# Performance work log

Hardware: AMD Instinct MI355X
Metric: run time of the kernel (lower is better)

## Reference

```python
import jax, jax.numpy as jnp
import numpy as np

NODE_DIM = 128
N_NODES = 100000
N_EDGES = 600000


def setup_inputs() -> dict:
    key = jax.random.key(0)
    k_x, k_e, k_w1, k_b1, k_w2, k_b2 = jax.random.split(key, 6)
    x = jax.random.normal(k_x, (N_NODES, NODE_DIM), dtype=jnp.float32)
    edge_index = jax.random.randint(k_e, (2, N_EDGES), 0, N_NODES, dtype=jnp.int64)
    # nn.Linear default init: U(-1/sqrt(fan_in), 1/sqrt(fan_in))
    lim1 = 1.0 / np.sqrt(2 * NODE_DIM)
    W1 = jax.random.uniform(k_w1, (2 * NODE_DIM, NODE_DIM), minval=-lim1, maxval=lim1, dtype=jnp.float32)
    b1 = jax.random.uniform(k_b1, (NODE_DIM,), minval=-lim1, maxval=lim1, dtype=jnp.float32)
    lim2 = 1.0 / np.sqrt(NODE_DIM)
    W2 = jax.random.uniform(k_w2, (NODE_DIM, 1), minval=-lim2, maxval=lim2, dtype=jnp.float32)
    b2 = jax.random.uniform(k_b2, (1,), minval=-lim2, maxval=lim2, dtype=jnp.float32)
    return {"x": x, "edge_index": edge_index, "W1": W1, "b1": b1, "W2": W2, "b2": b2}


def reference(x, edge_index, W1, b1, W2, b2):
    src = edge_index[0]
    dst = edge_index[1]
    # [E, 2*node_dim] gathered pair features
    pair = jnp.concatenate([x[src], x[dst]], axis=-1)
    h = jax.nn.relu(pair @ W1 + b1)          # [E, node_dim]
    s = jax.nn.sigmoid(h @ W2 + b2)          # [E, 1]
    return s.squeeze(-1)                      # [E]
```

## Files before the change

### kernel.cpp

```cpp
#include <hip/hip_runtime.h>
#include <hip/hip_bf16.h>
#include <stdint.h>

#define NODE_DIM 128
#define N_NODES  100000
#define N_EDGES  600000
#define NOUT     256

#define QSTEP_INV 64.0f
#define QSTEP     (1.0f / 64.0f)

typedef __bf16 bf16x8 __attribute__((ext_vector_type(8)));
typedef float  f32x4  __attribute__((ext_vector_type(4)));

static __device__ inline unsigned pack2_bf16(float a, float b) {
    unsigned short ua = __builtin_bit_cast(unsigned short, (__bf16)a);
    unsigned short ub = __builtin_bit_cast(unsigned short, (__bf16)b);
    return (unsigned)ua | ((unsigned)ub << 16);
}

static __device__ __forceinline__ void async_copy16(const void* g, void* l) {
    __builtin_amdgcn_global_load_lds(
        (__attribute__((address_space(1))) void*)(uintptr_t)g,
        (__attribute__((address_space(3))) void*)(uint32_t)(uintptr_t)l,
        16, 0, 0);
}

__global__ void wprep_kernel(const float* __restrict__ W1, __bf16* __restrict__ Wt) {
    int i = blockIdx.x * 256 + threadIdx.x;
    if (i >= NOUT * NODE_DIM) return;
    int kp = i >> 7;
    int n  = i & 127;
    float v = W1[i];
    int np = (kp < NODE_DIM) ? n  : (n + NODE_DIM);
    int k  = (kp < NODE_DIM) ? kp : (kp - NODE_DIM);
    Wt[np * NODE_DIM + k] = (__bf16)v;
}

#define MT     64
#define ELD    256
#define GB     512
#define NTILES 1563

__global__ __launch_bounds__(256)
void gemm_pre_kernel(const float* __restrict__ x, const __bf16* __restrict__ Wt,
                     const float* __restrict__ b1,
                     unsigned char* __restrict__ Ai, unsigned char* __restrict__ Bi) {
    __shared__ __align__(16) char lds_raw[2 * 32768];

    const int t    = threadIdx.x;
    const int wave = t >> 6;
    const int lane = t & 63;
    const int lm   = lane & 15;
    const int q    = lane >> 4;
    const int n0   = wave * 64;

    bf16x8 bfr[4][4];
#pragma unroll
    for (int nt = 0; nt < 4; ++nt) {
        const int n = n0 + nt * 16 + lm;
#pragma unroll
        for (int ks = 0; ks < 4; ++ks)
            bfr[nt][ks] = __builtin_bit_cast(bf16x8,
                *(const uint4*)(Wt + (size_t)n * NODE_DIM + ks * 32 + q * 8));
    }
    float bias[4];
#pragma unroll
    for (int nt = 0; nt < 4; ++nt) {
        const int n = n0 + nt * 16 + lm;
        bias[nt] = (n < NODE_DIM) ? b1[n] : 0.f;
    }

    auto STAGE = [&](int tile, int ib) {
        const int m0 = tile * MT;
#pragma unroll
        for (int i = 0; i < 8; ++i) {
            const int s     = i * 256 + wave * 64 + lane;
            const int sbase = i * 256 + wave * 64;
            const int R  = s >> 5;
            const int p  = s & 31;
            const int cg = p ^ (R & 7);
            int gr = m0 + R;
            if (gr > N_NODES - 1) gr = N_NODES - 1;
            async_copy16(x + (size_t)gr * NODE_DIM + cg * 4,
                         lds_raw + (size_t)(ib * 2048 + sbase) * 16);
        }
    };

    int tile = blockIdx.x;
    STAGE(tile, 0);
    asm volatile("s_waitcnt vmcnt(0)" ::: "memory");
    __builtin_amdgcn_s_barrier();

    int ib = 0;
    for (; tile < NTILES; tile += GB, ib ^= 1) {
        const int m0  = tile * MT;
        const int nxt = tile + GB;

        asm volatile("s_waitcnt lgkmcnt(0)" ::: "memory");
        __builtin_amdgcn_s_barrier();

        if (nxt < NTILES) {
            STAGE(nxt, ib ^ 1);
            asm volatile("s_waitcnt vmcnt(16)" ::: "memory");
        } else {
            asm volatile("s_waitcnt vmcnt(8)" ::: "memory");
        }
        __builtin_amdgcn_sched_barrier(0);
        __builtin_amdgcn_s_barrier();

        f32x4 acc[4][4];
#pragma unroll
        for (int a = 0; a < 4; ++a)
#pragma unroll
            for (int b = 0; b < 4; ++b)
                acc[a][b] = (f32x4){0.f, 0.f, 0.f, 0.f};

        const float* Xf = (const float*)(lds_raw + ib * 32768);
#pragma unroll
        for (int mt = 0; mt < 4; ++mt) {
            const int R  = mt * 16 + lm;
            const int rs = R & 7;
#pragma unroll
            for (int ks = 0; ks < 4; ++ks) {
                const int c0 = ks * 8 + q * 2;
                const float4 f0 = *(const float4*)&Xf[(R * 32 + (c0 ^ rs)) * 4];
                const float4 f1 = *(const float4*)&Xf[(R * 32 + ((c0 + 1) ^ rs)) * 4];
                uint4 p;
                p.x = pack2_bf16(f0.x, f0.y);
                p.y = pack2_bf16(f0.z, f0.w);
                p.z = pack2_bf16(f1.x, f1.y);
                p.w = pack2_bf16(f1.z, f1.w);
                bf16x8 af = __builtin_bit_cast(bf16x8, p);
#pragma unroll
                for (int nt = 0; nt < 4; ++nt)
                    acc[mt][nt] = __builtin_amdgcn_mfma_f32_16x16x32_bf16(
                        af, bfr[nt][ks], acc[mt][nt], 0, 0, 0);
            }
        }

        asm volatile("s_waitcnt lgkmcnt(0)" ::: "memory");
        __builtin_amdgcn_s_barrier();

        __bf16 (*Ls)[ELD] = (__bf16 (*)[ELD])(lds_raw + ib * 32768);
#pragma unroll
        for (int nt = 0; nt < 4; ++nt) {
            const int n = n0 + nt * 16 + lm;
#pragma unroll
            for (int mt = 0; mt < 4; ++mt) {
#pragma unroll
                for (int r = 0; r < 4; ++r)
                    Ls[mt * 16 + q * 4 + r][n] = (__bf16)(acc[mt][nt][r] + bias[nt]);
            }
        }
        asm volatile("s_waitcnt lgkmcnt(0)" ::: "memory");
        __builtin_amdgcn_s_barrier();

        const int grp = t >> 4;
        const int sub = t & 15;
#pragma unroll
        for (int pass = 0; pass < 8; ++pass) {
            const int hr   = pass * 16 + grp;
            const int row  = hr >> 1;
            const int half = hr & 1;
            const uint4 v = *(const uint4*)(&Ls[row][half * 128 + sub * 8]);
            const unsigned* vu = (const unsigned*)&v;
            unsigned u[8];
#pragma unroll
            for (int i = 0; i < 4; ++i) {
                const float fa = __builtin_bit_cast(float, vu[i] << 16);
                const float fb = __builtin_bit_cast(float, vu[i] & 0xffff0000u);
                float ga = fmaf(fa, QSTEP_INV, 128.5f);
                float gb = fmaf(fb, QSTEP_INV, 128.5f);
                ga = fminf(fmaxf(ga, 0.f), 255.f);
                gb = fminf(fmaxf(gb, 0.f), 255.f);
                u[2 * i]     = (unsigned)ga;
                u[2 * i + 1] = (unsigned)gb;
            }
            uint2 pk;
            pk.x = u[0] | (u[1] << 8) | (u[2] << 16) | (u[3] << 24);
            pk.y = u[4] | (u[5] << 8) | (u[6] << 16) | (u[7] << 24);
            int m = m0 + row;
            if (m > N_NODES - 1) m = N_NODES - 1;
            *(uint2*)((half ? Bi : Ai) + (size_t)m * NODE_DIM + sub * 8) = pk;
        }
    }
}

__global__ __launch_bounds__(256)
void edge_score_kernel(const unsigned char* __restrict__ Ai,
                       const unsigned char* __restrict__ Bi,
                       const int* __restrict__ idx,
                       const float* __restrict__ W2, const float* __restrict__ b2,
                       float* __restrict__ out) {
    const int t   = threadIdx.x;
    const int sub = t & 7;
    const int g   = (blockIdx.x * 256 + t) >> 3;
    const int e0  = g * 4;
    if (e0 >= N_EDGES) return;

    float w[16];
#pragma unroll
    for (int j = 0; j < 16; ++j) w[j] = W2[sub * 16 + j];
    const float bias2 = b2[0];

    const int4 sv = *(const int4*)(idx + e0);
    const int4 dv = *(const int4*)(idx + N_EDGES + e0);
    const int s[4] = {sv.x, sv.y, sv.z, sv.w};
    const int d[4] = {dv.x, dv.y, dv.z, dv.w};

    uint4 av[4], bv[4];
#pragma unroll
    for (int i = 0; i < 4; ++i) {
        av[i] = *(const uint4*)(Ai + (size_t)s[i] * NODE_DIM + sub * 16);
        bv[i] = *(const uint4*)(Bi + (size_t)d[i] * NODE_DIM + sub * 16);
    }

    float p[4];
#pragma unroll
    for (int i = 0; i < 4; ++i) {
        const unsigned aw[4] = {av[i].x, av[i].y, av[i].z, av[i].w};
        const unsigned bw[4] = {bv[i].x, bv[i].y, bv[i].z, bv[i].w};
        float acc = 0.f;
#pragma unroll
        for (int wd = 0; wd < 4; ++wd) {
#pragma unroll
            for (int k = 0; k < 4; ++k) {
                const int ua = (int)((aw[wd] >> (8 * k)) & 0xffu);
                const int ub = (int)((bw[wd] >> (8 * k)) & 0xffu);
                const int r  = max(ua + ub, 256) - 256;
                acc = fmaf((float)r, w[wd * 4 + k], acc);
            }
        }
        p[i] = acc;
    }

#pragma unroll
    for (int i = 0; i < 4; ++i) {
        p[i] += __shfl_xor(p[i], 1);
        p[i] += __shfl_xor(p[i], 2);
        p[i] += __shfl_xor(p[i], 4);
    }

    if (sub == 0) {
        float4 o;
        o.x = 1.f / (1.f + __expf(-fmaf(p[0], QSTEP, bias2)));
        o.y = 1.f / (1.f + __expf(-fmaf(p[1], QSTEP, bias2)));
        o.z = 1.f / (1.f + __expf(-fmaf(p[2], QSTEP, bias2)));
        o.w = 1.f / (1.f + __expf(-fmaf(p[3], QSTEP, bias2)));
        *(float4*)(out + e0) = o;
    }
}

__global__ __launch_bounds__(128)
void naive_edge_kernel(const float* __restrict__ x, const int* __restrict__ idx,
                       const float* __restrict__ W1, const float* __restrict__ b1,
                       const float* __restrict__ W2, const float* __restrict__ b2,
                       float* __restrict__ out) {
    __shared__ float pair[2 * NODE_DIM];
    __shared__ float red[2];
    int e = blockIdx.x;
    int t = threadIdx.x;
    int s = idx[e], d = idx[N_EDGES + e];
    pair[t]            = x[(size_t)s * NODE_DIM + t];
    pair[NODE_DIM + t] = x[(size_t)d * NODE_DIM + t];
    __syncthreads();
    float acc = b1[t];
    for (int k = 0; k < 2 * NODE_DIM; ++k)
        acc = fmaf(pair[k], W1[k * NODE_DIM + t], acc);
    float c = fmaxf(acc, 0.f) * W2[t];
#pragma unroll
    for (int m = 1; m < 64; m <<= 1) c += __shfl_xor(c, m);
    if ((t & 63) == 0) red[t >> 6] = c;
    __syncthreads();
    if (t == 0) out[e] = 1.f / (1.f + __expf(-(red[0] + red[1] + b2[0])));
}

extern "C" void kernel_launch(void* const* d_in, const int* in_sizes, int n_in,
                              void* d_out, int out_size, void* d_ws, size_t ws_size,
                              hipStream_t stream) {
    const float* x   = (const float*)d_in[0];
    const int*   idx = (const int*)d_in[1];
    const float* W1  = (const float*)d_in[2];
    const float* b1  = (const float*)d_in[3];
    const float* W2  = (const float*)d_in[4];
    const float* b2  = (const float*)d_in[5];
    float* out = (float*)d_out;

    const size_t tab_bytes = (size_t)N_NODES * NODE_DIM;
    const size_t wt_bytes  = (size_t)NOUT * NODE_DIM * sizeof(__bf16);
    const size_t need = 2 * tab_bytes + wt_bytes;

    if (ws_size >= need) {
        unsigned char* Ai = (unsigned char*)d_ws;
        unsigned char* Bi = Ai + tab_bytes;
        __bf16* Wt = (__bf16*)(Bi + tab_bytes);
        hipLaunchKernelGGL(wprep_kernel, dim3(128), dim3(256), 0, stream, W1, Wt);
        hipLaunchKernelGGL(gemm_pre_kernel, dim3(GB), dim3(256),
                           0, stream, x, Wt, b1, Ai, Bi);
        hipLaunchKernelGGL(edge_score_kernel, dim3((N_EDGES / 4 + 31) / 32), dim3(256),
                           0, stream, Ai, Bi, idx, W2, b2, out);
    } else {
        hipLaunchKernelGGL(naive_edge_kernel, dim3(N_EDGES), dim3(128), 0, stream,
                           x, idx, W1, b1, W2, b2, out);
    }
}
```

Baseline: 130.7 us.

## Quantize GEMM accumulators in registers and store directly, skipping LDS transpose

```diff
diff --git a/kernel.cpp b/kernel.cpp
--- a/kernel.cpp
+++ b/kernel.cpp
@@ -34,11 +34,11 @@
     float v = W1[i];
     int np = (kp < NODE_DIM) ? n  : (n + NODE_DIM);
     int k  = (kp < NODE_DIM) ? kp : (kp - NODE_DIM);
-    Wt[np * NODE_DIM + k] = (__bf16)v;
+    int npp = (np & ~0x3C) | ((np & 0x0C) << 2) | ((np & 0x30) >> 2);
+    Wt[npp * NODE_DIM + k] = (__bf16)v;
 }
 
 #define MT     64
-#define ELD    256
 #define GB     512
 #define NTILES 1563
 
@@ -64,11 +64,21 @@
             bfr[nt][ks] = __builtin_bit_cast(bf16x8,
                 *(const uint4*)(Wt + (size_t)n * NODE_DIM + ks * 32 + q * 8));
     }
-    float bias[4];
+
+    const int chbase = (n0 & 64) + q * 16;
+    unsigned char* __restrict__ Tbl = (n0 < NODE_DIM) ? Ai : Bi;
+    f32x4 bq[4];
 #pragma unroll
     for (int nt = 0; nt < 4; ++nt) {
-        const int n = n0 + nt * 16 + lm;
-        bias[nt] = (n < NODE_DIM) ? b1[n] : 0.f;
+        if (n0 < NODE_DIM) {
+            const float4 b = *(const float4*)(b1 + chbase + nt * 4);
+            bq[nt][0] = fmaf(b.x, QSTEP_INV, 128.5f);
+            bq[nt][1] = fmaf(b.y, QSTEP_INV, 128.5f);
+            bq[nt][2] = fmaf(b.z, QSTEP_INV, 128.5f);
+            bq[nt][3] = fmaf(b.w, QSTEP_INV, 128.5f);
+        } else {
+            bq[nt] = (f32x4){128.5f, 128.5f, 128.5f, 128.5f};
+        }
     }
 
     auto STAGE = [&](int tile, int ib) {
@@ -102,9 +112,9 @@
 
         if (nxt < NTILES) {
             STAGE(nxt, ib ^ 1);
-            asm volatile("s_waitcnt vmcnt(16)" ::: "memory");
+            asm volatile("s_waitcnt vmcnt(12)" ::: "memory");
         } else {
-            asm volatile("s_waitcnt vmcnt(8)" ::: "memory");
+            asm volatile("s_waitcnt vmcnt(4)" ::: "memory");
         }
         __builtin_amdgcn_sched_barrier(0);
         __builtin_amdgcn_s_barrier();
@@ -135,54 +145,29 @@
 #pragma unroll
                 for (int nt = 0; nt < 4; ++nt)
                     acc[mt][nt] = __builtin_amdgcn_mfma_f32_16x16x32_bf16(
-                        af, bfr[nt][ks], acc[mt][nt], 0, 0, 0);
+                        bfr[nt][ks], af, acc[mt][nt], 0, 0, 0);
             }
         }
 
-        asm volatile("s_waitcnt lgkmcnt(0)" ::: "memory");
-        __builtin_amdgcn_s_barrier();
-
-        __bf16 (*Ls)[ELD] = (__bf16 (*)[ELD])(lds_raw + ib * 32768);
-#pragma unroll
-        for (int nt = 0; nt < 4; ++nt) {
-            const int n = n0 + nt * 16 + lm;
-#pragma unroll
-            for (int mt = 0; mt < 4; ++mt) {
-#pragma unroll
-                for (int r = 0; r < 4; ++r)
-                    Ls[mt * 16 + q * 4 + r][n] = (__bf16)(acc[mt][nt][r] + bias[nt]);
+#pragma unroll
+        for (int mt = 0; mt < 4; ++mt) {
+            unsigned pw[4];
+#pragma unroll
+            for (int nt = 0; nt < 4; ++nt) {
+                unsigned u[4];
+#pragma unroll
+                for (int r = 0; r < 4; ++r) {
+                    float g = fmaf(acc[mt][nt][r], QSTEP_INV, bq[nt][r]);
+                    g = fminf(fmaxf(g, 0.f), 255.f);
+                    u[r] = (unsigned)g;
+                }
+                pw[nt] = u[0] | (u[1] << 8) | (u[2] << 16) | (u[3] << 24);
             }
-        }
-        asm volatile("s_waitcnt lgkmcnt(0)" ::: "memory");
-        __builtin_amdgcn_s_barrier();
-
-        const int grp = t >> 4;
-        const int sub = t & 15;
-#pragma unroll
-        for (int pass = 0; pass < 8; ++pass) {
-            const int hr   = pass * 16 + grp;
-            const int row  = hr >> 1;
-            const int half = hr & 1;
-            const uint4 v = *(const uint4*)(&Ls[row][half * 128 + sub * 8]);
-            const unsigned* vu = (const unsigned*)&v;
-            unsigned u[8];
-#pragma unroll
-            for (int i = 0; i < 4; ++i) {
-                const float fa = __builtin_bit_cast(float, vu[i] << 16);
-                const float fb = __builtin_bit_cast(float, vu[i] & 0xffff0000u);
-                float ga = fmaf(fa, QSTEP_INV, 128.5f);
-                float gb = fmaf(fb, QSTEP_INV, 128.5f);
-                ga = fminf(fmaxf(ga, 0.f), 255.f);
-                gb = fminf(fmaxf(gb, 0.f), 255.f);
-                u[2 * i]     = (unsigned)ga;
-                u[2 * i + 1] = (unsigned)gb;
-            }
-            uint2 pk;
-            pk.x = u[0] | (u[1] << 8) | (u[2] << 16) | (u[3] << 24);
-            pk.y = u[4] | (u[5] << 8) | (u[6] << 16) | (u[7] << 24);
-            int m = m0 + row;
+            uint4 pk;
+            pk.x = pw[0]; pk.y = pw[1]; pk.z = pw[2]; pk.w = pw[3];
+            int m = m0 + mt * 16 + lm;
             if (m > N_NODES - 1) m = N_NODES - 1;
-            *(uint2*)((half ? Bi : Ai) + (size_t)m * NODE_DIM + sub * 8) = pk;
+            *(uint4*)(Tbl + (size_t)m * NODE_DIM + chbase) = pk;
         }
     }
 }
```

New measurement: 127.6 us, median of 2. 2.4% less time.
